# Kernel optimization log

Measured on AMD Instinct MI355X. Metric: run time of the kernel, lower is better.

Reference implementation:

```python
import jax, jax.numpy as jnp
import numpy as np

B, HGT, WID, D, NS = 4, 64, 128, 128, 2
LN_EPS = 1e-5

def layer_norm(x, g, b):
    m = jnp.mean(x, axis=-1, keepdims=True)
    v = jnp.mean((x - m) ** 2, axis=-1, keepdims=True)
    return (x - m) * jax.lax.rsqrt(v + LN_EPS) * g + b

def setup_inputs() -> dict:
    key = jax.random.key(0)
    ks = jax.random.split(key, 8)
    src = jax.random.normal(ks[0], (B, HGT * WID, D), jnp.float32)
    L = (HGT // NS) * (WID // NS)  # 2048
    s = 0.05
    return {
        "source": src,
        "target": src,  # identical -> self-attention branch in original
        "shifted_window_attn_mask": jax.random.normal(ks[1], (NS * NS, L, L), jnp.float32),
        "shifted_window_attn_mask_1d": jnp.zeros((NS, WID // NS, WID // NS), jnp.float32),
        "height": HGT,
        "width": WID,
        "attn_num_splits": NS,
        "with_shift": 1,
        "Wq": jax.random.normal(ks[2], (D, D), jnp.float32) * s,
        "Wk": jax.random.normal(ks[3], (D, D), jnp.float32) * s,
        "Wv": jax.random.normal(ks[4], (D, D), jnp.float32) * s,
        "Wm": jax.random.normal(ks[5], (D, D), jnp.float32) * s,
        "g1": jnp.ones((D,), jnp.float32),
        "b1": jnp.zeros((D,), jnp.float32),
        "W1": jax.random.normal(ks[6], (2 * D, 8 * D), jnp.float32) * s,
        "W2": jax.random.normal(ks[7], (8 * D, D), jnp.float32) * s,
        "g2": jnp.ones((D,), jnp.float32),
        "b2": jnp.zeros((D,), jnp.float32),
    }

def _shifted_window_self_attn(q, k, v, ns, with_shift, h, w, attn_mask):
    b, _, c = q.shape
    hh, ww = h // ns, w // ns  # window sizes
    sh, sw = hh // 2, ww // 2
    L = hh * ww

    def to_windows(x):
        x = x.reshape(b, h, w, c)
        if with_shift:
            x = jnp.roll(x, shift=(-sh, -sw), axis=(1, 2))
        # (b, ns, hh, ns, ww, c) -> (b*ns*ns, hh*ww, c)
        x = x.reshape(b, ns, hh, ns, ww, c).transpose(0, 1, 3, 2, 4, 5)
        return x.reshape(b * ns * ns, L, c)

    qw, kw, vw = to_windows(q), to_windows(k), to_windows(v)
    scores = jnp.einsum("bqc,bkc->bqk", qw, kw) / (c ** 0.5)  # (b*ns^2, L, L)
    if with_shift:
        scores = (scores.reshape(b, ns * ns, L, L) + attn_mask).reshape(b * ns * ns, L, L)
    attn = jax.nn.softmax(scores, axis=-1)
    out = jnp.einsum("bqk,bkc->bqc", attn, vw)
    # merge windows back
    out = out.reshape(b, ns, ns, hh, ww, c).transpose(0, 1, 3, 2, 4, 5).reshape(b, h, w, c)
    if with_shift:
        out = jnp.roll(out, shift=(sh, sw), axis=(1, 2))
    return out.reshape(b, h * w, c)

def reference(source, target, shifted_window_attn_mask, shifted_window_attn_mask_1d,
              height, width, attn_num_splits, with_shift,
              Wq, Wk, Wv, Wm, g1, b1, W1, W2, g2, b2):
    # target == source -> self-attention, attn_num_splits > 1 -> shifted-window path
    q = source @ Wq
    k = target @ Wk
    v = target @ Wv
    message = _shifted_window_self_attn(q, k, v, attn_num_splits, with_shift,
                                        height, width, shifted_window_attn_mask)
    message = layer_norm(message @ Wm, g1, b1)
    h = jnp.concatenate([source, message], axis=-1)  # (B, HW, 2D)
    message = jax.nn.gelu(h @ W1, approximate=False) @ W2
    message = layer_norm(message, g2, b2)
    return source + message
```

## Files before the change

kernel.cpp:

```cpp
#include <hip/hip_runtime.h>

typedef unsigned short u16;
typedef __bf16 bf16x8 __attribute__((ext_vector_type(8)));
typedef float f32x4 __attribute__((ext_vector_type(4)));

#define MFMA(a, b, c) __builtin_amdgcn_mfma_f32_16x16x32_bf16(a, b, c, 0, 0, 0)


__device__ __forceinline__ u16 f2b(float f) {
  unsigned u = __builtin_bit_cast(unsigned, f);
  u += 0x7fffu + ((u >> 16) & 1u);
  return (u16)(u >> 16);
}
__device__ __forceinline__ float b2f(u16 h) {
  unsigned u = (unsigned)h << 16;
  return __builtin_bit_cast(float, u);
}
__device__ __forceinline__ void glds16(const u16* g, u16* l) {
  __builtin_amdgcn_global_load_lds((const __attribute__((address_space(1))) void*)g,
                                   (__attribute__((address_space(3))) void*)l, 16, 0, 0);
}

#define QW_OFF   ((size_t)0)
#define KW_OFF   ((size_t)8 << 20)
#define VBUF_OFF ((size_t)16 << 20)
#define O1_OFF   ((size_t)24 << 20)
#define O2_OFF   ((size_t)40 << 20)
#define HID_OFF  ((size_t)0)
#define SRCB_OFF ((size_t)64 << 20)
#define MSG1_OFF ((size_t)72 << 20)
#define L1_OFF   ((size_t)80 << 20)
#define L2P_OFF  (((size_t)80 << 20) + 131072)
#define WQT_OFF  (((size_t)80 << 20) + 262144)
#define WKT_OFF  (WQT_OFF + 32768)
#define WVT_OFF  (WQT_OFF + 65536)
#define WMT_OFF  (WQT_OFF + 98304)
#define W1T_OFF  (WQT_OFF + 131072)
#define W2T_OFF  (WQT_OFF + 655360)

__global__ void k_prep(const float* __restrict__ wq, const float* __restrict__ wk,
                       const float* __restrict__ wv, const float* __restrict__ wm,
                       const float* __restrict__ w1, const float* __restrict__ w2,
                       u16* __restrict__ wqt, u16* __restrict__ wkt,
                       u16* __restrict__ wvt, u16* __restrict__ wmt,
                       u16* __restrict__ w1t, u16* __restrict__ w2t) {
  int t = blockIdx.x * 256 + threadIdx.x;
  if (t < 65536) {
    int m = t >> 14, loc = t & 16383;
    int n = loc >> 7, k = loc & 127;
    const float* s = (m == 0) ? wq : (m == 1) ? wk : (m == 2) ? wv : wm;
    u16* d = (m == 0) ? wqt : (m == 1) ? wkt : (m == 2) ? wvt : wmt;
    const float sc = (m == 0) ? 0.08838834764831845f : 1.0f;
    d[n * 128 + k] = f2b(s[k * 128 + n] * sc);
  } else if (t < 65536 + 262144) {
    int loc = t - 65536;
    int n = loc >> 8, k = loc & 255;
    w1t[n * 256 + k] = f2b(w1[k * 1024 + n]);
  } else if (t < 65536 + 262144 + 131072) {
    int loc = t - 327680;
    int n = loc >> 10, k = loc & 1023;
    w2t[n * 1024 + k] = f2b(w2[k * 128 + n]);
  }
}

__global__ __launch_bounds__(256, 2)
void k_qkv(const float* __restrict__ src,
           const u16* __restrict__ wtq, const u16* __restrict__ wtk,
           const u16* __restrict__ wtv,
           u16* __restrict__ qw, u16* __restrict__ kw, u16* __restrict__ vbuf,
           u16* __restrict__ srcb) {
  __shared__ __align__(16) u16 At[64 * 136];
  __shared__ __align__(16) u16 Bt[128 * 136];
  const int tid = threadIdx.x, bid = blockIdx.x;
  const int lane = tid & 63, wid = tid >> 6;
  const int l15 = lane & 15, quad = lane >> 4;

  {
    const int row = tid >> 2, part = tid & 3;
    const int t = bid * 64 + row;
    const int g = t >> 11, p = t & 2047;
    const int b = g >> 2, wi = (g >> 1) & 1, wj = g & 1;
    const int ii = p >> 6, jj = p & 63;
    const int y = (wi * 32 + ii + 16) & 63;
    const int x = (wj * 64 + jj + 32) & 127;
    const int srow = b * 8192 + y * 128 + x;
    const float4* sp = (const float4*)(src + srow * 128) + part * 8;
    u16* lp = &At[row * 136 + part * 32];
    u16* gp = srcb + srow * 128 + part * 32;
#pragma unroll
    for (int q = 0; q < 8; ++q) {
      float4 v = sp[q];
      ushort4 h = make_ushort4(f2b(v.x), f2b(v.y), f2b(v.z), f2b(v.w));
      *(ushort4*)(lp + q * 4) = h;
      *(ushort4*)(gp + q * 4) = h;
    }
  }
  __syncthreads();

  bf16x8 afrag[4];
  const int arow = wid * 16 + l15;
#pragma unroll
  for (int kk = 0; kk < 4; ++kk)
    afrag[kk] = *(const bf16x8*)&At[arow * 136 + kk * 32 + quad * 8];

  const f32x4 fz = {0.f, 0.f, 0.f, 0.f};
#pragma unroll 1
  for (int m = 0; m < 3; ++m) {
    const u16* wp = (m == 0) ? wtq : (m == 1) ? wtk : wtv;
    {
      const int n = tid >> 1, half = tid & 1;
      const uint4* sp = (const uint4*)(wp + n * 128 + half * 64);
      uint4* dp = (uint4*)&Bt[n * 136 + half * 64];
#pragma unroll
      for (int q = 0; q < 8; ++q) dp[q] = sp[q];
    }
    __syncthreads();
    f32x4 acc[8];
#pragma unroll
    for (int nt = 0; nt < 8; ++nt) acc[nt] = fz;
#pragma unroll
    for (int kk = 0; kk < 4; ++kk) {
#pragma unroll
      for (int nt = 0; nt < 8; ++nt) {
        bf16x8 bfr = *(const bf16x8*)&Bt[(nt * 16 + l15) * 136 + kk * 32 + quad * 8];
        acc[nt] = MFMA(afrag[kk], bfr, acc[nt]);
      }
    }
    const int t0 = bid * 64 + wid * 16 + quad * 4;
    if (m < 2) {
      u16* dst = (m == 0) ? qw : kw;
#pragma unroll
      for (int nt = 0; nt < 8; ++nt) {
        const int d = nt * 16 + l15;
#pragma unroll
        for (int r = 0; r < 4; ++r) dst[(t0 + r) * 128 + d] = f2b(acc[nt][r]);
      }
    } else {
      const int g = bid >> 5;
      const int p0 = t0 & 2047;
#pragma unroll
      for (int nt = 0; nt < 8; ++nt) {
        const int d = nt * 16 + l15;
        ushort4 hv = make_ushort4(f2b(acc[nt][0]), f2b(acc[nt][1]),
                                  f2b(acc[nt][2]), f2b(acc[nt][3]));
        *(ushort4*)&vbuf[g * 262144 + d * 2048 + p0] = hv;
      }
    }
    __syncthreads();
  }
}

__global__ __launch_bounds__(256, 3)
void k_attn(const u16* __restrict__ qw, const u16* __restrict__ kw,
            const u16* __restrict__ vbuf, const float* __restrict__ mask,
            u16* __restrict__ o1, u16* __restrict__ o2,
            float* __restrict__ l1, float* __restrict__ l2) {
  __shared__ __align__(16) u16 Kt[64 * 128];
  __shared__ __align__(16) u16 Vt[128 * 64];
  __shared__ __align__(16) u16 Pt[64 * 72];
  const int tid = threadIdx.x, bid = blockIdx.x;
  const int lane = tid & 63, wid = tid >> 6;
  const int l15 = lane & 15, quad = lane >> 4;
  const int b = bid & 3, w = (bid >> 2) & 3, half = (bid >> 4) & 1, qb = bid >> 5;
  const int g = b * 4 + w;
  const int k0 = half * 1024;
  const u16* kbase = kw + g * 262144 + k0 * 128;
  const u16* vbase = vbuf + g * 262144 + k0;
  const int qrow0 = qb * 64 + wid * 16 + quad * 4;
  const float* mlane = mask + (size_t)w * 4194304 + (size_t)qrow0 * 2048 + k0 + l15;

  int offk[4], offv[4];
#pragma unroll
  for (int j = 0; j < 4; ++j) {
    const int s = wid * 256 + j * 64 + lane;
    const int r = s >> 4, cbk = (s & 15) ^ (r & 15);
    offk[j] = r * 128 + cbk * 8;
    const int d = s >> 3, cbv = (s & 7) ^ (d & 7);
    offv[j] = d * 2048 + cbv * 8;
  }

  bf16x8 qfrag[4];
  {
    const u16* qp = qw + g * 262144 + (qb * 64 + wid * 16 + l15) * 128 + quad * 8;
#pragma unroll
    for (int kk = 0; kk < 4; ++kk) qfrag[kk] = *(const bf16x8*)(qp + kk * 32);
  }
  const f32x4 fz = {0.f, 0.f, 0.f, 0.f};
  f32x4 o[8];
#pragma unroll
  for (int nt = 0; nt < 8; ++nt) o[nt] = fz;
  float lr[4] = {0.f, 0.f, 0.f, 0.f};
  const float L2E = 1.4426950408889634f;

  float mpf[16];
#pragma unroll
  for (int nt = 0; nt < 4; ++nt)
#pragma unroll
    for (int r = 0; r < 4; ++r) mpf[nt * 4 + r] = mlane[r * 2048 + nt * 16];

#pragma unroll 1
  for (int kt = 0; kt < 16; ++kt) {
    __syncthreads();
#pragma unroll
    for (int j = 0; j < 4; ++j)
      glds16(kbase + kt * 8192 + offk[j], &Kt[wid * 2048 + j * 512]);
#pragma unroll
    for (int j = 0; j < 4; ++j)
      glds16(vbase + kt * 64 + offv[j], &Vt[wid * 2048 + j * 512]);
    float mn[16];
    if (kt < 15) {
#pragma unroll
      for (int nt = 0; nt < 4; ++nt)
#pragma unroll
        for (int r = 0; r < 4; ++r)
          mn[nt * 4 + r] = mlane[r * 2048 + (kt + 1) * 64 + nt * 16];
    }
    __syncthreads();

    f32x4 s[4];
#pragma unroll
    for (int nt = 0; nt < 4; ++nt)
#pragma unroll
      for (int r = 0; r < 4; ++r) s[nt][r] = mpf[nt * 4 + r];
#pragma unroll
    for (int kk = 0; kk < 4; ++kk)
#pragma unroll
      for (int nt = 0; nt < 4; ++nt) {
        bf16x8 bfr = *(const bf16x8*)&Kt[(nt * 16 + l15) * 128 +
                                         (((kk * 4 + quad) ^ l15) * 8)];
        s[nt] = MFMA(qfrag[kk], bfr, s[nt]);
      }
#pragma unroll
    for (int nt = 0; nt < 4; ++nt)
#pragma unroll
      for (int r = 0; r < 4; ++r) {
        const float pv = exp2f(s[nt][r] * L2E);
        lr[r] += pv;
        Pt[(wid * 16 + quad * 4 + r) * 72 + nt * 16 + l15] = f2b(pv);
      }
    bf16x8 pfrag[2];
#pragma unroll
    for (int kkp = 0; kkp < 2; ++kkp)
      pfrag[kkp] = *(const bf16x8*)&Pt[(wid * 16 + l15) * 72 + kkp * 32 + quad * 8];
#pragma unroll
    for (int nt = 0; nt < 8; ++nt)
#pragma unroll
      for (int kkp = 0; kkp < 2; ++kkp) {
        bf16x8 bfr = *(const bf16x8*)&Vt[(nt * 16 + l15) * 64 +
                                         (((kkp * 4 + quad) ^ (l15 & 7)) * 8)];
        o[nt] = MFMA(pfrag[kkp], bfr, o[nt]);
      }
    if (kt < 15) {
#pragma unroll
      for (int i = 0; i < 16; ++i) mpf[i] = mn[i];
    }
  }

#pragma unroll
  for (int off = 1; off < 16; off <<= 1)
#pragma unroll
    for (int r = 0; r < 4; ++r) lr[r] += __shfl_xor(lr[r], off, 16);
  u16* op = half ? o2 : o1;
  float* lp = half ? l2 : l1;
  const int t0 = g * 2048 + qrow0;
#pragma unroll
  for (int r = 0; r < 4; ++r) {
    const float inv = 1.f / lr[r];
#pragma unroll
    for (int nt = 0; nt < 8; ++nt)
      op[(size_t)(t0 + r) * 128 + nt * 16 + l15] = f2b(o[nt][r] * inv);
    if (l15 == 0) lp[t0 + r] = lr[r];
  }
}

__global__ __launch_bounds__(256, 2)
void k_wmln(const u16* __restrict__ o1, const u16* __restrict__ o2,
            const float* __restrict__ l1, const float* __restrict__ l2,
            const u16* __restrict__ wmt, const float* __restrict__ g1,
            const float* __restrict__ b1, u16* __restrict__ msg1) {
  __shared__ __align__(16) u16 At[64 * 136];
  __shared__ __align__(16) u16 Bt[128 * 136];
  const int tid = threadIdx.x, bid = blockIdx.x;
  const int lane = tid & 63, wid = tid >> 6;
  const int l15 = lane & 15, quad = lane >> 4;
  {
    const int row = tid >> 2, part = tid & 3;
    const int m = bid * 64 + row;
    const float la = l1[m], lb = l2[m];
    const float wA = la / (la + lb), wB = lb / (la + lb);
    const u16* p1 = o1 + (size_t)m * 128 + part * 32;
    const u16* p2 = o2 + (size_t)m * 128 + part * 32;
    u16* lp = &At[row * 136 + part * 32];
#pragma unroll
    for (int q = 0; q < 4; ++q) {
      ushort4 xa = *(const ushort4*)(p1 + q * 8);
      ushort4 xb = *(const ushort4*)(p1 + q * 8 + 4);
      ushort4 ya = *(const ushort4*)(p2 + q * 8);
      ushort4 yb = *(const ushort4*)(p2 + q * 8 + 4);
      ushort4 ha = make_ushort4(f2b(b2f(xa.x) * wA + b2f(ya.x) * wB),
                                f2b(b2f(xa.y) * wA + b2f(ya.y) * wB),
                                f2b(b2f(xa.z) * wA + b2f(ya.z) * wB),
                                f2b(b2f(xa.w) * wA + b2f(ya.w) * wB));
      ushort4 hb = make_ushort4(f2b(b2f(xb.x) * wA + b2f(yb.x) * wB),
                                f2b(b2f(xb.y) * wA + b2f(yb.y) * wB),
                                f2b(b2f(xb.z) * wA + b2f(yb.z) * wB),
                                f2b(b2f(xb.w) * wA + b2f(yb.w) * wB));
      *(ushort4*)(lp + q * 8) = ha;
      *(ushort4*)(lp + q * 8 + 4) = hb;
    }
  }
  {
    const int n = tid >> 1, half = tid & 1;
    const uint4* sp = (const uint4*)(wmt + n * 128 + half * 64);
    uint4* dp = (uint4*)&Bt[n * 136 + half * 64];
#pragma unroll
    for (int q = 0; q < 8; ++q) dp[q] = sp[q];
  }
  __syncthreads();
  bf16x8 afrag[4];
  const int arow = wid * 16 + l15;
#pragma unroll
  for (int kk = 0; kk < 4; ++kk)
    afrag[kk] = *(const bf16x8*)&At[arow * 136 + kk * 32 + quad * 8];
  const f32x4 fz = {0.f, 0.f, 0.f, 0.f};
  f32x4 acc[8];
#pragma unroll
  for (int nt = 0; nt < 8; ++nt) acc[nt] = fz;
#pragma unroll
  for (int kk = 0; kk < 4; ++kk)
#pragma unroll
    for (int nt = 0; nt < 8; ++nt) {
      bf16x8 bfr = *(const bf16x8*)&Bt[(nt * 16 + l15) * 136 + kk * 32 + quad * 8];
      acc[nt] = MFMA(afrag[kk], bfr, acc[nt]);
    }
  float sum[4] = {0, 0, 0, 0}, sq[4] = {0, 0, 0, 0};
#pragma unroll
  for (int nt = 0; nt < 8; ++nt)
#pragma unroll
    for (int r = 0; r < 4; ++r) {
      const float v = acc[nt][r];
      sum[r] += v;
      sq[r] += v * v;
    }
#pragma unroll
  for (int off = 1; off < 16; off <<= 1)
#pragma unroll
    for (int r = 0; r < 4; ++r) {
      sum[r] += __shfl_xor(sum[r], off, 16);
      sq[r] += __shfl_xor(sq[r], off, 16);
    }
  float mean[4], rstd[4];
#pragma unroll
  for (int r = 0; r < 4; ++r) {
    mean[r] = sum[r] * (1.f / 128.f);
    const float var = sq[r] * (1.f / 128.f) - mean[r] * mean[r];
    rstd[r] = rsqrtf(var + 1e-5f);
  }
  const int t0 = bid * 64 + wid * 16 + quad * 4;
#pragma unroll
  for (int nt = 0; nt < 8; ++nt) {
    const int d = nt * 16 + l15;
    const float gg = g1[d], bb = b1[d];
#pragma unroll
    for (int r = 0; r < 4; ++r) {
      const int tt = t0 + r;
      const int gw = tt >> 11, pp = tt & 2047;
      const int bb2 = gw >> 2, wi = (gw >> 1) & 1, wj = gw & 1;
      const int ii = pp >> 6, jj = pp & 63;
      const int yy = (wi * 32 + ii + 16) & 63;
      const int xx = (wj * 64 + jj + 32) & 127;
      msg1[(bb2 * 8192 + yy * 128 + xx) * 128 + d] =
          f2b((acc[nt][r] - mean[r]) * rstd[r] * gg + bb);
    }
  }
}

__global__ __launch_bounds__(256, 3)
void k_mlp1(const u16* __restrict__ srcb, const u16* __restrict__ msg1,
            const u16* __restrict__ w1t, u16* __restrict__ hid) {
  __shared__ __align__(16) u16 At[64 * 72];
  __shared__ __align__(16) u16 Bt[256 * 72];
  const int tid = threadIdx.x, bid = blockIdx.x;
  const int rb = bid >> 2, nb = bid & 3;
  const int lane = tid & 63, wid = tid >> 6;
  const int l15 = lane & 15, quad = lane >> 4;
  const f32x4 fz = {0.f, 0.f, 0.f, 0.f};
  f32x4 acc[16];
#pragma unroll
  for (int nt = 0; nt < 16; ++nt) acc[nt] = fz;
#pragma unroll 1
  for (int kc = 0; kc < 4; ++kc) {
    __syncthreads();
    {
      const int row = tid >> 2, part = tid & 3;
      const u16* sp0 = (kc < 2) ? srcb : msg1;
      const uint4* sp = (const uint4*)(sp0 + (rb * 64 + row) * 128 + (kc & 1) * 64 + part * 16);
      uint4* dp = (uint4*)&At[row * 72 + part * 16];
      dp[0] = sp[0];
      dp[1] = sp[1];
    }
    {
      const uint4* sp = (const uint4*)(w1t + (nb * 256 + tid) * 256 + kc * 64);
      uint4* dp = (uint4*)&Bt[tid * 72];
#pragma unroll
      for (int q = 0; q < 8; ++q) dp[q] = sp[q];
    }
    __syncthreads();
#pragma unroll
    for (int kk = 0; kk < 2; ++kk) {
      bf16x8 a = *(const bf16x8*)&At[(wid * 16 + l15) * 72 + kk * 32 + quad * 8];
#pragma unroll
      for (int nt = 0; nt < 16; ++nt) {
        bf16x8 b = *(const bf16x8*)&Bt[(nt * 16 + l15) * 72 + kk * 32 + quad * 8];
        acc[nt] = MFMA(a, b, acc[nt]);
      }
    }
  }
  const int t0 = rb * 64 + wid * 16 + quad * 4;
#pragma unroll
  for (int nt = 0; nt < 16; ++nt) {
    const int n = nb * 256 + nt * 16 + l15;
#pragma unroll
    for (int r = 0; r < 4; ++r) {
      const float x = acc[nt][r];
      const float y = 0.5f * x * (1.f + erff(x * 0.70710678118654752f));
      hid[(size_t)(t0 + r) * 1024 + n] = f2b(y);
    }
  }
}

__global__ __launch_bounds__(256, 2)
void k_mlp2(const u16* __restrict__ hid, const u16* __restrict__ w2t,
            const float* __restrict__ g2, const float* __restrict__ b2,
            const float* __restrict__ src, float* __restrict__ out) {
  __shared__ __align__(16) u16 At[64 * 72];
  __shared__ __align__(16) u16 Bt[128 * 72];
  const int tid = threadIdx.x, bid = blockIdx.x;
  const int lane = tid & 63, wid = tid >> 6;
  const int l15 = lane & 15, quad = lane >> 4;
  const f32x4 fz = {0.f, 0.f, 0.f, 0.f};
  f32x4 acc[8];
#pragma unroll
  for (int nt = 0; nt < 8; ++nt) acc[nt] = fz;
#pragma unroll 1
  for (int kc = 0; kc < 16; ++kc) {
    __syncthreads();
    {
      const int row = tid >> 2, part = tid & 3;
      const uint4* sp = (const uint4*)(hid + (size_t)(bid * 64 + row) * 1024 + kc * 64 + part * 16);
      uint4* dp = (uint4*)&At[row * 72 + part * 16];
      dp[0] = sp[0];
      dp[1] = sp[1];
    }
    {
      const int n = tid >> 1, half = tid & 1;
      const uint4* sp = (const uint4*)(w2t + n * 1024 + kc * 64 + half * 32);
      uint4* dp = (uint4*)&Bt[n * 72 + half * 32];
#pragma unroll
      for (int q = 0; q < 4; ++q) dp[q] = sp[q];
    }
    __syncthreads();
#pragma unroll
    for (int kk = 0; kk < 2; ++kk) {
      bf16x8 a = *(const bf16x8*)&At[(wid * 16 + l15) * 72 + kk * 32 + quad * 8];
#pragma unroll
      for (int nt = 0; nt < 8; ++nt) {
        bf16x8 b = *(const bf16x8*)&Bt[(nt * 16 + l15) * 72 + kk * 32 + quad * 8];
        acc[nt] = MFMA(a, b, acc[nt]);
      }
    }
  }
  float sum[4] = {0, 0, 0, 0}, sq[4] = {0, 0, 0, 0};
#pragma unroll
  for (int nt = 0; nt < 8; ++nt)
#pragma unroll
    for (int r = 0; r < 4; ++r) {
      const float v = acc[nt][r];
      sum[r] += v;
      sq[r] += v * v;
    }
#pragma unroll
  for (int off = 1; off < 16; off <<= 1)
#pragma unroll
    for (int r = 0; r < 4; ++r) {
      sum[r] += __shfl_xor(sum[r], off, 16);
      sq[r] += __shfl_xor(sq[r], off, 16);
    }
  float mean[4], rstd[4];
#pragma unroll
  for (int r = 0; r < 4; ++r) {
    mean[r] = sum[r] * (1.f / 128.f);
    const float var = sq[r] * (1.f / 128.f) - mean[r] * mean[r];
    rstd[r] = rsqrtf(var + 1e-5f);
  }
  const int t0 = bid * 64 + wid * 16 + quad * 4;
#pragma unroll
  for (int nt = 0; nt < 8; ++nt) {
    const int d = nt * 16 + l15;
    const float gg = g2[d], bb = b2[d];
#pragma unroll
    for (int r = 0; r < 4; ++r) {
      const int idx = (t0 + r) * 128 + d;
      out[idx] = src[idx] + (acc[nt][r] - mean[r]) * rstd[r] * gg + bb;
    }
  }
}

extern "C" void kernel_launch(void* const* d_in, const int* in_sizes, int n_in,
                              void* d_out, int out_size, void* d_ws, size_t ws_size,
                              hipStream_t stream) {
  const float* src  = (const float*)d_in[0];
  const float* mask = (const float*)d_in[2];
  const float* Wq = (const float*)d_in[8];
  const float* Wk = (const float*)d_in[9];
  const float* Wv = (const float*)d_in[10];
  const float* Wm = (const float*)d_in[11];
  const float* g1 = (const float*)d_in[12];
  const float* b1 = (const float*)d_in[13];
  const float* W1 = (const float*)d_in[14];
  const float* W2 = (const float*)d_in[15];
  const float* g2 = (const float*)d_in[16];
  const float* b2 = (const float*)d_in[17];
  char* ws = (char*)d_ws;
  u16* qw   = (u16*)(ws + QW_OFF);
  u16* kw   = (u16*)(ws + KW_OFF);
  u16* vbuf = (u16*)(ws + VBUF_OFF);
  u16* o1   = (u16*)(ws + O1_OFF);
  u16* o2   = (u16*)(ws + O2_OFF);
  float* l1 = (float*)(ws + L1_OFF);
  float* l2 = (float*)(ws + L2P_OFF);
  u16* hid  = (u16*)(ws + HID_OFF);
  u16* srcb = (u16*)(ws + SRCB_OFF);
  u16* msg1 = (u16*)(ws + MSG1_OFF);
  u16* wqt = (u16*)(ws + WQT_OFF);
  u16* wkt = (u16*)(ws + WKT_OFF);
  u16* wvt = (u16*)(ws + WVT_OFF);
  u16* wmt = (u16*)(ws + WMT_OFF);
  u16* w1t = (u16*)(ws + W1T_OFF);
  u16* w2t = (u16*)(ws + W2T_OFF);

  k_prep<<<1792, 256, 0, stream>>>(Wq, Wk, Wv, Wm, W1, W2, wqt, wkt, wvt, wmt, w1t, w2t);
  k_qkv<<<512, 256, 0, stream>>>(src, wqt, wkt, wvt, qw, kw, vbuf, srcb);
  k_attn<<<1024, 256, 0, stream>>>(qw, kw, vbuf, mask, o1, o2, l1, l2);
  k_wmln<<<512, 256, 0, stream>>>(o1, o2, l1, l2, wmt, g1, b1, msg1);
  k_mlp1<<<2048, 256, 0, stream>>>(srcb, msg1, w1t, hid);
  k_mlp2<<<512, 256, 0, stream>>>(hid, w2t, g2, b2, src, (float*)d_out);
}
```

Before: 341.0 us.

## Double-buffer K/V tiles in attention kernel and raise occupancy to four blocks

The attention kernel now processes 32-key tiles instead of 64-key tiles. It keeps two LDS buffers for K and V, prefetching the next tile asynchronously while computing on the current one, and syncing once per iteration instead of twice. The smaller P staging buffer and tiles keep total LDS within a budget that lets launch bounds ask for four resident blocks per CU. In exchange there are twice as many loop iterations with less MFMA work each, plus more barrier and loop overhead per key.

```diff
diff --git a/kernel.cpp b/kernel.cpp
--- a/kernel.cpp
+++ b/kernel.cpp
@@ -150,14 +150,14 @@
   }
 }
 
-__global__ __launch_bounds__(256, 3)
+__global__ __launch_bounds__(256, 4)
 void k_attn(const u16* __restrict__ qw, const u16* __restrict__ kw,
             const u16* __restrict__ vbuf, const float* __restrict__ mask,
             u16* __restrict__ o1, u16* __restrict__ o2,
             float* __restrict__ l1, float* __restrict__ l2) {
-  __shared__ __align__(16) u16 Kt[64 * 128];
-  __shared__ __align__(16) u16 Vt[128 * 64];
-  __shared__ __align__(16) u16 Pt[64 * 72];
+  __shared__ __align__(16) u16 Kt[2][32 * 128];
+  __shared__ __align__(16) u16 Vt[2][128 * 32];
+  __shared__ __align__(16) u16 Pt[64 * 40];
   const int tid = threadIdx.x, bid = blockIdx.x;
   const int lane = tid & 63, wid = tid >> 6;
   const int l15 = lane & 15, quad = lane >> 4;
@@ -169,14 +169,15 @@
   const int qrow0 = qb * 64 + wid * 16 + quad * 4;
   const float* mlane = mask + (size_t)w * 4194304 + (size_t)qrow0 * 2048 + k0 + l15;
 
-  int offk[4], offv[4];
-#pragma unroll
-  for (int j = 0; j < 4; ++j) {
-    const int s = wid * 256 + j * 64 + lane;
-    const int r = s >> 4, cbk = (s & 15) ^ (r & 15);
-    offk[j] = r * 128 + cbk * 8;
-    const int d = s >> 3, cbv = (s & 7) ^ (d & 7);
-    offv[j] = d * 2048 + cbv * 8;
+  int offk[2], offv[2], dstb[2];
+#pragma unroll
+  for (int j = 0; j < 2; ++j) {
+    const int s = wid * 128 + j * 64 + lane;
+    const int rk = s >> 4, bk = (s & 15) ^ (rk & 15);
+    offk[j] = rk * 128 + bk * 8;
+    const int dv = s >> 2, bv = (s & 3) ^ (dv & 3);
+    offv[j] = dv * 2048 + bv * 8;
+    dstb[j] = (wid * 128 + j * 64) * 8;
   }
 
   bf16x8 qfrag[4];
@@ -192,67 +193,70 @@
   float lr[4] = {0.f, 0.f, 0.f, 0.f};
   const float L2E = 1.4426950408889634f;
 
-  float mpf[16];
-#pragma unroll
-  for (int nt = 0; nt < 4; ++nt)
+#pragma unroll
+  for (int j = 0; j < 2; ++j) {
+    glds16(kbase + offk[j], &Kt[0][dstb[j]]);
+    glds16(vbase + offv[j], &Vt[0][dstb[j]]);
+  }
+  float mpf[8];
+#pragma unroll
+  for (int nt = 0; nt < 2; ++nt)
 #pragma unroll
     for (int r = 0; r < 4; ++r) mpf[nt * 4 + r] = mlane[r * 2048 + nt * 16];
 
 #pragma unroll 1
-  for (int kt = 0; kt < 16; ++kt) {
-    __syncthreads();
-#pragma unroll
-    for (int j = 0; j < 4; ++j)
-      glds16(kbase + kt * 8192 + offk[j], &Kt[wid * 2048 + j * 512]);
-#pragma unroll
-    for (int j = 0; j < 4; ++j)
-      glds16(vbase + kt * 64 + offv[j], &Vt[wid * 2048 + j * 512]);
-    float mn[16];
-    if (kt < 15) {
-#pragma unroll
-      for (int nt = 0; nt < 4; ++nt)
+  for (int kt = 0; kt < 32; ++kt) {
+    const int p = kt & 1;
+    __syncthreads();
+    if (kt < 31) {
+      const u16* kb = kbase + (kt + 1) * 4096;
+      const u16* vb = vbase + (kt + 1) * 32;
+#pragma unroll
+      for (int j = 0; j < 2; ++j) {
+        glds16(kb + offk[j], &Kt[p ^ 1][dstb[j]]);
+        glds16(vb + offv[j], &Vt[p ^ 1][dstb[j]]);
+      }
+    }
+    float mn[8];
+    if (kt < 31) {
+#pragma unroll
+      for (int nt = 0; nt < 2; ++nt)
 #pragma unroll
         for (int r = 0; r < 4; ++r)
-          mn[nt * 4 + r] = mlane[r * 2048 + (kt + 1) * 64 + nt * 16];
-    }
-    __syncthreads();
-
-    f32x4 s[4];
-#pragma unroll
-    for (int nt = 0; nt < 4; ++nt)
+          mn[nt * 4 + r] = mlane[r * 2048 + (kt + 1) * 32 + nt * 16];
+    }
+
+    f32x4 s[2];
+#pragma unroll
+    for (int nt = 0; nt < 2; ++nt)
 #pragma unroll
       for (int r = 0; r < 4; ++r) s[nt][r] = mpf[nt * 4 + r];
 #pragma unroll
     for (int kk = 0; kk < 4; ++kk)
 #pragma unroll
-      for (int nt = 0; nt < 4; ++nt) {
-        bf16x8 bfr = *(const bf16x8*)&Kt[(nt * 16 + l15) * 128 +
-                                         (((kk * 4 + quad) ^ l15) * 8)];
+      for (int nt = 0; nt < 2; ++nt) {
+        bf16x8 bfr = *(const bf16x8*)&Kt[p][(nt * 16 + l15) * 128 +
+                                           (((kk * 4 + quad) ^ l15) * 8)];
         s[nt] = MFMA(qfrag[kk], bfr, s[nt]);
       }
 #pragma unroll
-    for (int nt = 0; nt < 4; ++nt)
+    for (int nt = 0; nt < 2; ++nt)
 #pragma unroll
       for (int r = 0; r < 4; ++r) {
         const float pv = exp2f(s[nt][r] * L2E);
         lr[r] += pv;
-        Pt[(wid * 16 + quad * 4 + r) * 72 + nt * 16 + l15] = f2b(pv);
-      }
-    bf16x8 pfrag[2];
-#pragma unroll
-    for (int kkp = 0; kkp < 2; ++kkp)
-      pfrag[kkp] = *(const bf16x8*)&Pt[(wid * 16 + l15) * 72 + kkp * 32 + quad * 8];
-#pragma unroll
-    for (int nt = 0; nt < 8; ++nt)
-#pragma unroll
-      for (int kkp = 0; kkp < 2; ++kkp) {
-        bf16x8 bfr = *(const bf16x8*)&Vt[(nt * 16 + l15) * 64 +
-                                         (((kkp * 4 + quad) ^ (l15 & 7)) * 8)];
-        o[nt] = MFMA(pfrag[kkp], bfr, o[nt]);
-      }
-    if (kt < 15) {
-#pragma unroll
-      for (int i = 0; i < 16; ++i) mpf[i] = mn[i];
+        Pt[(wid * 16 + quad * 4 + r) * 40 + nt * 16 + l15] = f2b(pv);
+      }
+    bf16x8 pfrag = *(const bf16x8*)&Pt[(wid * 16 + l15) * 40 + quad * 8];
+#pragma unroll
+    for (int nt = 0; nt < 8; ++nt) {
+      bf16x8 bfr = *(const bf16x8*)&Vt[p][(nt * 16 + l15) * 32 +
+                                          ((quad ^ (l15 & 3)) * 8)];
+      o[nt] = MFMA(pfrag, bfr, o[nt]);
+    }
+    if (kt < 31) {
+#pragma unroll
+      for (int i = 0; i < 8; ++i) mpf[i] = mn[i];
     }
   }
 
```

Result: faster. 333.1 us (-2.3%).
